# Performance work log

Measured on AMD Instinct MI355X. Metric: run time of the kernel, lower is better.

Reference implementation:

```python
import jax, jax.numpy as jnp
import numpy as np

B, C, N = 32, 128, 64
HID = 2 * C
STEEPNESS = 50.0


def _bitonic_layers(n):
    """Index pairs (a, b) for each compare-exchange layer of a bitonic sorting
    network, matching diffsort's bitonic_network construction."""
    num_blocks = int(np.log2(n))
    assert n == 2 ** num_blocks
    layers = []
    for block in range(num_blocks):
        for layer in range(block + 1):
            m = 2 ** (block - layer)
            a_idx, b_idx = [], []
            for i in range(0, n, 2 * m):
                for j in range(m):
                    ix = i + j
                    a, b = ix, ix + m
                    # alternate direction within bitonic blocks
                    if (ix // 2 ** (block + 1)) % 2 == 1:
                        a, b = b, a
                    a_idx.append(a)
                    b_idx.append(b)
            layers.append((np.asarray(a_idx), np.asarray(b_idx)))
    return layers

_LAYERS = _bitonic_layers(N)  # 21 layers for N=64


def _diff_sort(scores):
    """Differentiable bitonic sort (diffsort, distribution='cauchy').
    Returns (soft-sorted scores, soft permutation matrix P) with
    sorted = scores @ P; the module applies P via bmm(P, rows)."""
    b, n = scores.shape
    x = scores
    P = jnp.broadcast_to(jnp.eye(n, dtype=scores.dtype), (b, n, n))
    inv_pi = 1.0 / np.pi
    for a_idx, b_idx in _LAYERS:
        xa, xb = x[:, a_idx], x[:, b_idx]
        alpha = jnp.arctan((xb - xa) * STEEPNESS) * inv_pi + 0.5  # Cauchy CDF
        x = x.at[:, a_idx].set(alpha * xa + (1.0 - alpha) * xb)
        x = x.at[:, b_idx].set((1.0 - alpha) * xa + alpha * xb)
        Pa, Pb = P[:, :, a_idx], P[:, :, b_idx]
        al = alpha[:, None, :]
        P = P.at[:, :, a_idx].set(al * Pa + (1.0 - al) * Pb)
        P = P.at[:, :, b_idx].set((1.0 - al) * Pa + al * Pb)
    return x, P


def setup_inputs() -> dict:
    key = jax.random.key(0)
    ks = jax.random.split(key, 9)
    s = 0.05  # keep score magnitudes reasonable under steepness=50
    return {
        "x": jax.random.normal(ks[0], (B, C, N, N), jnp.float32),
        "w1": jax.random.normal(ks[1], (HID, C), jnp.float32) * s,
        "b1": jax.random.normal(ks[2], (HID,), jnp.float32) * s,
        "w2": jax.random.normal(ks[3], (HID, HID), jnp.float32) * s,
        "b2": jax.random.normal(ks[4], (HID,), jnp.float32) * s,
        "w_row": jax.random.normal(ks[5], (HID, N), jnp.float32) * s,
        "b_row": jax.random.normal(ks[6], (1,), jnp.float32) * s,
        "w_col": jax.random.normal(ks[7], (HID, N), jnp.float32) * s,
        "b_col": jax.random.normal(ks[8], (1,), jnp.float32) * s,
    }


def reference(x, w1, b1, w2, b2, w_row, b_row, w_col, b_col):
    # feat_extractor: two 1x1 convs (pointwise channel GEMMs) + ReLU
    h = jax.nn.relu(jnp.einsum('bchw,oc->bohw', x, w1) + b1[None, :, None, None])
    h = jax.nn.relu(jnp.einsum('bchw,oc->bohw', h, w2) + b2[None, :, None, None])

    # row branch: Conv1d(HID*N,1,1) over flattened (channel, width) per row
    row_scores = jnp.einsum('bchw,cw->bh', h, w_row) + b_row  # (B, N)
    _, p_row = _diff_sort(row_scores)
    x = jnp.einsum('bij,bcjk->bcik', p_row, x)  # bmm(P_row, x) per channel

    # col branch: Conv1d(HID*N,1,1) over flattened (channel, height) per column
    col_scores = jnp.einsum('bchw,ch->bw', h, w_col) + b_col  # (B, N)
    _, p_col = _diff_sort(col_scores)
    # original: bmm(P_col, x^T) then view as (B,C,N,N) with NO transpose back
    x = jnp.einsum('bij,bckj->bcik', p_col, x)
    return x
```

## Files before the change

### kernel.cpp

```cpp
#include <hip/hip_runtime.h>
#include <math.h>

#define B_    32
#define C_    128
#define N_    64
#define HID_  256
#define PIX_  4096
#define STEEP 50.0f
#define INV_PI 0.318309886183790671f
#define LDA   40
#define LDX   72

typedef unsigned short u16;
typedef __attribute__((ext_vector_type(8))) short bf16x8;
typedef __attribute__((ext_vector_type(4))) float f32x4;

__device__ __forceinline__ u16 f2bf(float f) {
    unsigned int u = __builtin_bit_cast(unsigned int, f);
    unsigned int r = (u + 0x7FFFu + ((u >> 16) & 1u)) >> 16;
    return (u16)r;
}
__device__ __forceinline__ float bf2f(u16 h) {
    unsigned int u = ((unsigned int)h) << 16;
    return __builtin_bit_cast(float, u);
}

__global__ void k0_init(float* __restrict__ row_s, float* __restrict__ col_s,
                        const float* __restrict__ b_row, const float* __restrict__ b_col) {
    int i = blockIdx.x * 256 + threadIdx.x;
    if (i < B_ * N_) row_s[i] = b_row[0];
    else {
        int j = i - B_ * N_;
        if (j < B_ * N_) col_s[j] = b_col[0];
    }
}

__global__ void k_prep(const float* __restrict__ w1, const float* __restrict__ w2,
                       u16* __restrict__ w1h, u16* __restrict__ w1l,
                       u16* __restrict__ w2h, u16* __restrict__ w2l) {
    int i = blockIdx.x * 256 + threadIdx.x;
    if (i < HID_ * C_) {
        float v = w1[i];
        u16 h = f2bf(v);
        w1h[i] = h;
        w1l[i] = f2bf(v - bf2f(h));
    } else {
        int j = i - HID_ * C_;
        if (j < HID_ * HID_) {
            float v = w2[j];
            u16 h = f2bf(v);
            w2h[j] = h;
            w2l[j] = f2bf(v - bf2f(h));
        }
    }
}

__global__ __launch_bounds__(256) void k1_conv1(const float* __restrict__ x,
                                                const u16* __restrict__ w1h,
                                                const u16* __restrict__ w1l,
                                                const float* __restrict__ b1,
                                                u16* __restrict__ h1h,
                                                u16* __restrict__ h1l) {
    __shared__ __align__(16) u16 Ah[128 * LDA];
    __shared__ __align__(16) u16 Al[128 * LDA];
    __shared__ __align__(16) u16 Bh[128 * LDA];
    __shared__ __align__(16) u16 Bl[128 * LDA];
    const int t = threadIdx.x;
    const int l = t & 63, wv = t >> 6;
    const int row = l & 15, q = l >> 4;
    const int pbase = blockIdx.x * 128, obase = blockIdx.y * 128, b = blockIdx.z;
    const int mwave = (wv & 1) * 64, nwave = (wv >> 1) * 64;
    const float* xb = x + (size_t)b * C_ * PIX_ + pbase;

    f32x4 acc[4][4];
#pragma unroll
    for (int i = 0; i < 4; i++)
#pragma unroll
        for (int j = 0; j < 4; j++) acc[i][j] = (f32x4){0.f, 0.f, 0.f, 0.f};

    for (int k0 = 0; k0 < C_; k0 += 32) {
        {
            int o = t >> 1, hf = t & 1;
            const float4* sh = (const float4*)&w1h[(size_t)(obase + o) * C_ + k0 + hf * 16];
            const float4* sl = (const float4*)&w1l[(size_t)(obase + o) * C_ + k0 + hf * 16];
            float4 vh0 = sh[0], vh1 = sh[1];
            float4 vl0 = sl[0], vl1 = sl[1];
            *(float4*)&Ah[o * LDA + hf * 16] = vh0;
            *(float4*)&Ah[o * LDA + hf * 16 + 8] = vh1;
            *(float4*)&Al[o * LDA + hf * 16] = vl0;
            *(float4*)&Al[o * LDA + hf * 16 + 8] = vl1;
        }
        {
            int cp = t & 15, pg = t >> 4;
            int c = k0 + cp * 2;
            float4 a0 = *(const float4*)&xb[(size_t)c * PIX_ + pg * 8];
            float4 a1 = *(const float4*)&xb[(size_t)c * PIX_ + pg * 8 + 4];
            float4 c0v = *(const float4*)&xb[(size_t)(c + 1) * PIX_ + pg * 8];
            float4 c1v = *(const float4*)&xb[(size_t)(c + 1) * PIX_ + pg * 8 + 4];
            float va[8] = {a0.x, a0.y, a0.z, a0.w, a1.x, a1.y, a1.z, a1.w};
            float vb[8] = {c0v.x, c0v.y, c0v.z, c0v.w, c1v.x, c1v.y, c1v.z, c1v.w};
#pragma unroll
            for (int j = 0; j < 8; j++) {
                u16 h0 = f2bf(va[j]), h1v = f2bf(vb[j]);
                u16 l0 = f2bf(va[j] - bf2f(h0)), l1 = f2bf(vb[j] - bf2f(h1v));
                *(unsigned int*)&Bh[(pg * 8 + j) * LDA + cp * 2] =
                    (unsigned int)h0 | ((unsigned int)h1v << 16);
                *(unsigned int*)&Bl[(pg * 8 + j) * LDA + cp * 2] =
                    (unsigned int)l0 | ((unsigned int)l1 << 16);
            }
        }
        __syncthreads();

        bf16x8 afh[4], afl[4], bfh[4], bfl[4];
#pragma unroll
        for (int mf = 0; mf < 4; mf++) {
            afh[mf] = *(const bf16x8*)&Ah[(mwave + mf * 16 + row) * LDA + q * 8];
            afl[mf] = *(const bf16x8*)&Al[(mwave + mf * 16 + row) * LDA + q * 8];
        }
#pragma unroll
        for (int nf = 0; nf < 4; nf++) {
            bfh[nf] = *(const bf16x8*)&Bh[(nwave + nf * 16 + row) * LDA + q * 8];
            bfl[nf] = *(const bf16x8*)&Bl[(nwave + nf * 16 + row) * LDA + q * 8];
        }
#pragma unroll
        for (int mf = 0; mf < 4; mf++)
#pragma unroll
            for (int nf = 0; nf < 4; nf++) {
                acc[mf][nf] = __builtin_amdgcn_mfma_f32_16x16x32_bf16(afh[mf], bfh[nf], acc[mf][nf], 0, 0, 0);
                acc[mf][nf] = __builtin_amdgcn_mfma_f32_16x16x32_bf16(afh[mf], bfl[nf], acc[mf][nf], 0, 0, 0);
                acc[mf][nf] = __builtin_amdgcn_mfma_f32_16x16x32_bf16(afl[mf], bfh[nf], acc[mf][nf], 0, 0, 0);
            }
        __syncthreads();
    }

#pragma unroll
    for (int mf = 0; mf < 4; mf++) {
        int o = obase + mwave + mf * 16 + q * 4;
        float bias[4];
#pragma unroll
        for (int r = 0; r < 4; r++) bias[r] = b1[o + r];
#pragma unroll
        for (int nf = 0; nf < 4; nf++) {
            int p = pbase + nwave + nf * 16 + row;
            u16 hh[4], ll[4];
#pragma unroll
            for (int r = 0; r < 4; r++) {
                float v = fmaxf(acc[mf][nf][r] + bias[r], 0.f);
                u16 h = f2bf(v);
                hh[r] = h;
                ll[r] = f2bf(v - bf2f(h));
            }
            size_t base = ((size_t)b * PIX_ + p) * HID_ + o;
            *(unsigned long long*)&h1h[base] =
                (unsigned long long)hh[0] | ((unsigned long long)hh[1] << 16) |
                ((unsigned long long)hh[2] << 32) | ((unsigned long long)hh[3] << 48);
            *(unsigned long long*)&h1l[base] =
                (unsigned long long)ll[0] | ((unsigned long long)ll[1] << 16) |
                ((unsigned long long)ll[2] << 32) | ((unsigned long long)ll[3] << 48);
        }
    }
}

__global__ __launch_bounds__(256) void k2_conv2_scores(
    const u16* __restrict__ h1h, const u16* __restrict__ h1l,
    const u16* __restrict__ w2h, const u16* __restrict__ w2l,
    const float* __restrict__ b2, const float* __restrict__ w_row,
    const float* __restrict__ w_col, float* __restrict__ row_s,
    float* __restrict__ col_s) {
    __shared__ __align__(16) u16 Ah[128 * LDA];
    __shared__ __align__(16) u16 Al[128 * LDA];
    __shared__ __align__(16) u16 Bh[128 * LDA];
    __shared__ __align__(16) u16 Bl[128 * LDA];
    __shared__ float col_red[64];
    __shared__ float row_red[2];
    const int t = threadIdx.x;
    const int l = t & 63, wv = t >> 6;
    const int row = l & 15, q = l >> 4;
    const int pbase = blockIdx.x * 128, obase = blockIdx.y * 128, b = blockIdx.z;
    const int mwave = (wv & 1) * 64, nwave = (wv >> 1) * 64;

    if (t < 64) col_red[t] = 0.f;
    if (t < 2) row_red[t] = 0.f;

    f32x4 acc[4][4];
#pragma unroll
    for (int i = 0; i < 4; i++)
#pragma unroll
        for (int j = 0; j < 4; j++) acc[i][j] = (f32x4){0.f, 0.f, 0.f, 0.f};

    for (int k0 = 0; k0 < HID_; k0 += 32) {
        {
            int o = t >> 1, hf = t & 1;
            const float4* sh = (const float4*)&w2h[(size_t)(obase + o) * HID_ + k0 + hf * 16];
            const float4* sl = (const float4*)&w2l[(size_t)(obase + o) * HID_ + k0 + hf * 16];
            float4 vh0 = sh[0], vh1 = sh[1];
            float4 vl0 = sl[0], vl1 = sl[1];
            *(float4*)&Ah[o * LDA + hf * 16] = vh0;
            *(float4*)&Ah[o * LDA + hf * 16 + 8] = vh1;
            *(float4*)&Al[o * LDA + hf * 16] = vl0;
            *(float4*)&Al[o * LDA + hf * 16 + 8] = vl1;
        }
        {
            int p = t >> 1, hf = t & 1;
            size_t base = ((size_t)b * PIX_ + pbase + p) * HID_ + k0 + hf * 16;
            const float4* sh = (const float4*)&h1h[base];
            const float4* sl = (const float4*)&h1l[base];
            float4 vh0 = sh[0], vh1 = sh[1];
            float4 vl0 = sl[0], vl1 = sl[1];
            *(float4*)&Bh[p * LDA + hf * 16] = vh0;
            *(float4*)&Bh[p * LDA + hf * 16 + 8] = vh1;
            *(float4*)&Bl[p * LDA + hf * 16] = vl0;
            *(float4*)&Bl[p * LDA + hf * 16 + 8] = vl1;
        }
        __syncthreads();

        bf16x8 afh[4], afl[4], bfh[4], bfl[4];
#pragma unroll
        for (int mf = 0; mf < 4; mf++) {
            afh[mf] = *(const bf16x8*)&Ah[(mwave + mf * 16 + row) * LDA + q * 8];
            afl[mf] = *(const bf16x8*)&Al[(mwave + mf * 16 + row) * LDA + q * 8];
        }
#pragma unroll
        for (int nf = 0; nf < 4; nf++) {
            bfh[nf] = *(const bf16x8*)&Bh[(nwave + nf * 16 + row) * LDA + q * 8];
            bfl[nf] = *(const bf16x8*)&Bl[(nwave + nf * 16 + row) * LDA + q * 8];
        }
#pragma unroll
        for (int mf = 0; mf < 4; mf++)
#pragma unroll
            for (int nf = 0; nf < 4; nf++) {
                acc[mf][nf] = __builtin_amdgcn_mfma_f32_16x16x32_bf16(afh[mf], bfh[nf], acc[mf][nf], 0, 0, 0);
                acc[mf][nf] = __builtin_amdgcn_mfma_f32_16x16x32_bf16(afh[mf], bfl[nf], acc[mf][nf], 0, 0, 0);
                acc[mf][nf] = __builtin_amdgcn_mfma_f32_16x16x32_bf16(afl[mf], bfh[nf], acc[mf][nf], 0, 0, 0);
            }
        __syncthreads();
    }

    const int h0 = pbase >> 6;
    const int h = h0 + (wv >> 1);
    float rpart = 0.f;
    float cpart[4] = {0.f, 0.f, 0.f, 0.f};
#pragma unroll
    for (int mf = 0; mf < 4; mf++) {
        int o = obase + mwave + mf * 16 + q * 4;
#pragma unroll
        for (int r = 0; r < 4; r++) {
            float bias = b2[o + r];
            float wcv = w_col[(o + r) * N_ + h];
#pragma unroll
            for (int nf = 0; nf < 4; nf++) {
                int w = nf * 16 + row;
                float v = fmaxf(acc[mf][nf][r] + bias, 0.f);
                rpart += v * w_row[(o + r) * N_ + w];
                cpart[nf] += v * wcv;
            }
        }
    }
    __syncthreads();
#pragma unroll
    for (int off = 32; off; off >>= 1) rpart += __shfl_xor(rpart, off, 64);
    if (l == 0) atomicAdd(&row_red[wv >> 1], rpart);
#pragma unroll
    for (int nf = 0; nf < 4; nf++) {
        float cp = cpart[nf];
        cp += __shfl_xor(cp, 16, 64);
        cp += __shfl_xor(cp, 32, 64);
        if (l < 16) atomicAdd(&col_red[nf * 16 + l], cp);
    }
    __syncthreads();
    if (t < 64) atomicAdd(&col_s[b * N_ + t], col_red[t]);
    if (t < 2) atomicAdd(&row_s[b * N_ + h0 + t], row_red[t]);
}

__global__ __launch_bounds__(256) void k4_diffsort(const float* __restrict__ row_s,
                                                   const float* __restrict__ col_s,
                                                   u16* __restrict__ prow_h, u16* __restrict__ prow_l,
                                                   u16* __restrict__ pcol_h, u16* __restrict__ pcol_l) {
    __shared__ float Ps[64 * 65];
    __shared__ float xs[64];
    __shared__ float als[32];
    const int t = threadIdx.x;
    const int which = blockIdx.x & 1;
    const int b = blockIdx.x >> 1;
    const float* sc = which ? col_s : row_s;
    u16* Ph = which ? pcol_h : prow_h;
    u16* Pl = which ? pcol_l : prow_l;

    if (t < 64) xs[t] = sc[b * 64 + t];
#pragma unroll
    for (int k = 0; k < 16; k++) {
        int idx = t + k * 256;
        int i = idx >> 6, j = idx & 63;
        Ps[i * 65 + j] = (i == j) ? 1.f : 0.f;
    }
    __syncthreads();

    const int r = t & 63, pg = t >> 6;
    for (int bl = 0; bl < 6; bl++) {
        for (int ly = 0; ly <= bl; ly++) {
            int sh = bl - ly;
            int m = 1 << sh;
            if (t < 32) {
                int i = (t >> sh) << (sh + 1);
                int j = t & (m - 1);
                int ix = i + j;
                int a = ix, bi = ix + m;
                if ((ix >> (bl + 1)) & 1) { int tmp = a; a = bi; bi = tmp; }
                float xa = xs[a], xbv = xs[bi];
                float al = atanf((xbv - xa) * STEEP) * INV_PI + 0.5f;
                als[t] = al;
                xs[a] = al * xa + (1.f - al) * xbv;
                xs[bi] = (1.f - al) * xa + al * xbv;
            }
            __syncthreads();
#pragma unroll
            for (int pi = 0; pi < 8; pi++) {
                int p = pg * 8 + pi;
                int i = (p >> sh) << (sh + 1);
                int j = p & (m - 1);
                int ix = i + j;
                int a = ix, bi = ix + m;
                if ((ix >> (bl + 1)) & 1) { int tmp = a; a = bi; bi = tmp; }
                float al = als[p];
                float Pa = Ps[r * 65 + a], Pb = Ps[r * 65 + bi];
                Ps[r * 65 + a] = al * Pa + (1.f - al) * Pb;
                Ps[r * 65 + bi] = (1.f - al) * Pa + al * Pb;
            }
            __syncthreads();
        }
    }
#pragma unroll
    for (int k = 0; k < 16; k++) {
        int idx = t + k * 256;
        int i = idx >> 6, j = idx & 63;
        float v = Ps[i * 65 + j];
        u16 h = f2bf(v);
        Ph[b * 4096 + idx] = h;
        Pl[b * 4096 + idx] = f2bf(v - bf2f(h));
    }
}

__global__ __launch_bounds__(256) void k5_permute(const float* __restrict__ x,
                                                  const u16* __restrict__ pcol_h,
                                                  const u16* __restrict__ pcol_l,
                                                  const u16* __restrict__ prow_h,
                                                  const u16* __restrict__ prow_l,
                                                  float* __restrict__ out) {
    __shared__ __align__(16) u16 Xh[64 * LDX];
    __shared__ __align__(16) u16 Xl[64 * LDX];
    __shared__ __align__(16) u16 Zh[64 * LDX];
    __shared__ __align__(16) u16 Zl[64 * LDX];
    const int t = threadIdx.x;
    const int l = t & 63, w = t >> 6;
    const int col = l & 15, q = l >> 4;
    const int b = blockIdx.y;
    const int cbase = blockIdx.x * 4;
    const int i0 = w * 16;

    const u16* pch = pcol_h + (size_t)b * 4096;
    const u16* pcl = pcol_l + (size_t)b * 4096;
    const u16* prh = prow_h + (size_t)b * 4096;
    const u16* prl = prow_l + (size_t)b * 4096;

    bf16x8 pcA_h[2], pcA_l[2];
#pragma unroll
    for (int ks = 0; ks < 2; ks++) {
        pcA_h[ks] = *(const bf16x8*)&pch[(i0 + col) * 64 + q * 8 + ks * 32];
        pcA_l[ks] = *(const bf16x8*)&pcl[(i0 + col) * 64 + q * 8 + ks * 32];
    }

    for (int ci = 0; ci < 4; ci++) {
        const int c = cbase + ci;
        const float* xc = x + ((size_t)b * C_ + c) * PIX_;
#pragma unroll
        for (int k = 0; k < 4; k++) {
            int f = t + k * 256;
            int rw = f >> 4, c4 = f & 15;
            float4 v = *(const float4*)&xc[f * 4];
            u16 h0 = f2bf(v.x), h1 = f2bf(v.y), h2 = f2bf(v.z), h3 = f2bf(v.w);
            ushort4 hv = {h0, h1, h2, h3};
            ushort4 lv = {f2bf(v.x - bf2f(h0)), f2bf(v.y - bf2f(h1)),
                          f2bf(v.z - bf2f(h2)), f2bf(v.w - bf2f(h3))};
            *(ushort4*)&Xh[rw * LDX + c4 * 4] = hv;
            *(ushort4*)&Xl[rw * LDX + c4 * 4] = lv;
        }
        __syncthreads();

        f32x4 acc[4];
#pragma unroll
        for (int nt = 0; nt < 4; nt++) acc[nt] = (f32x4){0.f, 0.f, 0.f, 0.f};
#pragma unroll
        for (int ks = 0; ks < 2; ks++) {
            bf16x8 ah = pcA_h[ks], al_ = pcA_l[ks];
#pragma unroll
            for (int nt = 0; nt < 4; nt++) {
                bf16x8 bh = *(const bf16x8*)&Xh[(nt * 16 + col) * LDX + q * 8 + ks * 32];
                bf16x8 bl = *(const bf16x8*)&Xl[(nt * 16 + col) * LDX + q * 8 + ks * 32];
                acc[nt] = __builtin_amdgcn_mfma_f32_16x16x32_bf16(ah, bh, acc[nt], 0, 0, 0);
                acc[nt] = __builtin_amdgcn_mfma_f32_16x16x32_bf16(ah, bl, acc[nt], 0, 0, 0);
                acc[nt] = __builtin_amdgcn_mfma_f32_16x16x32_bf16(al_, bh, acc[nt], 0, 0, 0);
            }
        }
#pragma unroll
        for (int nt = 0; nt < 4; nt++)
#pragma unroll
            for (int r = 0; r < 4; r++) {
                float v = acc[nt][r];
                u16 h = f2bf(v);
                int rw = i0 + q * 4 + r;
                Zh[rw * LDX + nt * 16 + col] = h;
                Zl[rw * LDX + nt * 16 + col] = f2bf(v - bf2f(h));
            }

        f32x4 acc2[4];
#pragma unroll
        for (int nt = 0; nt < 4; nt++) acc2[nt] = (f32x4){0.f, 0.f, 0.f, 0.f};
#pragma unroll
        for (int ks = 0; ks < 2; ks++) {
            bf16x8 ah = *(const bf16x8*)&Zh[(i0 + col) * LDX + q * 8 + ks * 32];
            bf16x8 al_ = *(const bf16x8*)&Zl[(i0 + col) * LDX + q * 8 + ks * 32];
#pragma unroll
            for (int nt = 0; nt < 4; nt++) {
                bf16x8 bh = *(const bf16x8*)&prh[(nt * 16 + col) * 64 + q * 8 + ks * 32];
                bf16x8 bl = *(const bf16x8*)&prl[(nt * 16 + col) * 64 + q * 8 + ks * 32];
                acc2[nt] = __builtin_amdgcn_mfma_f32_16x16x32_bf16(ah, bh, acc2[nt], 0, 0, 0);
                acc2[nt] = __builtin_amdgcn_mfma_f32_16x16x32_bf16(ah, bl, acc2[nt], 0, 0, 0);
                acc2[nt] = __builtin_amdgcn_mfma_f32_16x16x32_bf16(al_, bh, acc2[nt], 0, 0, 0);
            }
        }
        float* oc = out + ((size_t)b * C_ + c) * PIX_;
#pragma unroll
        for (int nt = 0; nt < 4; nt++)
#pragma unroll
            for (int r = 0; r < 4; r++)
                oc[(i0 + q * 4 + r) * 64 + nt * 16 + col] = acc2[nt][r];
        __syncthreads();
    }
}

extern "C" void kernel_launch(void* const* d_in, const int* in_sizes, int n_in,
                              void* d_out, int out_size, void* d_ws, size_t ws_size,
                              hipStream_t stream) {
    const float* x = (const float*)d_in[0];
    const float* w1 = (const float*)d_in[1];
    const float* b1 = (const float*)d_in[2];
    const float* w2 = (const float*)d_in[3];
    const float* b2 = (const float*)d_in[4];
    const float* w_row = (const float*)d_in[5];
    const float* b_row = (const float*)d_in[6];
    const float* w_col = (const float*)d_in[7];
    const float* b_col = (const float*)d_in[8];
    float* out = (float*)d_out;

    char* ws = (char*)d_ws;
    u16* h1h = (u16*)(ws);
    u16* h1l = (u16*)(ws + 67108864);
    u16* w1h = (u16*)(ws + 134217728);
    u16* w1l = (u16*)(ws + 134283264);
    u16* w2h = (u16*)(ws + 134348800);
    u16* w2l = (u16*)(ws + 134479872);
    float* row_s = (float*)(ws + 134610944);
    float* col_s = (float*)(ws + 134619136);
    u16* prow_h = (u16*)(ws + 134627328);
    u16* prow_l = (u16*)(ws + 134889472);
    u16* pcol_h = (u16*)(ws + 135151616);
    u16* pcol_l = (u16*)(ws + 135413760);

    hipLaunchKernelGGL(k0_init, dim3(16), dim3(256), 0, stream, row_s, col_s, b_row, b_col);
    hipLaunchKernelGGL(k_prep, dim3(384), dim3(256), 0, stream, w1, w2, w1h, w1l, w2h, w2l);
    hipLaunchKernelGGL(k1_conv1, dim3(32, 2, 32), dim3(256), 0, stream, x, w1h, w1l, b1, h1h, h1l);
    hipLaunchKernelGGL(k2_conv2_scores, dim3(32, 2, 32), dim3(256), 0, stream,
                       h1h, h1l, w2h, w2l, b2, w_row, w_col, row_s, col_s);
    hipLaunchKernelGGL(k4_diffsort, dim3(64), dim3(256), 0, stream,
                       row_s, col_s, prow_h, prow_l, pcol_h, pcol_l);
    hipLaunchKernelGGL(k5_permute, dim3(32, 32), dim3(256), 0, stream,
                       x, pcol_h, pcol_l, prow_h, prow_l, out);
}
```

Measured before the change: 320.2 us.

## Fuse conv1 and conv2+scores into one kernel keeping h1 in LDS

Merges the two pointwise-conv GEMM kernels into one. Each block handles one image row (64 pixels) across all 256 hidden channels and keeps the split-bf16 intermediate h1 in shared memory, so the 128 MB global write and read of h1 is removed. Weights are now read straight from global memory into MFMA fragments instead of being staged in LDS. Each block computes its row score whole, so the row-score init and its atomics are dropped. The cost is about 70 KB of LDS per block, which lowers occupancy, plus uncached-through-LDS weight loads.

```diff
diff --git a/kernel.cpp b/kernel.cpp
--- a/kernel.cpp
+++ b/kernel.cpp
@@ -9,6 +9,7 @@
 #define STEEP 50.0f
 #define INV_PI 0.318309886183790671f
 #define LDA   40
+#define LDH   272
 #define LDX   72
 
 typedef unsigned short u16;
@@ -25,14 +26,9 @@
     return __builtin_bit_cast(float, u);
 }
 
-__global__ void k0_init(float* __restrict__ row_s, float* __restrict__ col_s,
-                        const float* __restrict__ b_row, const float* __restrict__ b_col) {
+__global__ void k0_init(float* __restrict__ col_s, const float* __restrict__ b_col) {
     int i = blockIdx.x * 256 + threadIdx.x;
-    if (i < B_ * N_) row_s[i] = b_row[0];
-    else {
-        int j = i - B_ * N_;
-        if (j < B_ * N_) col_s[j] = b_col[0];
-    }
+    if (i < B_ * N_) col_s[i] = b_col[0];
 }
 
 __global__ void k_prep(const float* __restrict__ w1, const float* __restrict__ w2,
@@ -55,221 +51,170 @@
     }
 }
 
-__global__ __launch_bounds__(256) void k1_conv1(const float* __restrict__ x,
-                                                const u16* __restrict__ w1h,
-                                                const u16* __restrict__ w1l,
-                                                const float* __restrict__ b1,
-                                                u16* __restrict__ h1h,
-                                                u16* __restrict__ h1l) {
-    __shared__ __align__(16) u16 Ah[128 * LDA];
-    __shared__ __align__(16) u16 Al[128 * LDA];
-    __shared__ __align__(16) u16 Bh[128 * LDA];
-    __shared__ __align__(16) u16 Bl[128 * LDA];
+__global__ __launch_bounds__(256) void k12_fused(
+    const float* __restrict__ x,
+    const u16* __restrict__ w1h, const u16* __restrict__ w1l,
+    const float* __restrict__ b1,
+    const u16* __restrict__ w2h, const u16* __restrict__ w2l,
+    const float* __restrict__ b2, const float* __restrict__ w_row,
+    const float* __restrict__ b_row, const float* __restrict__ w_col,
+    float* __restrict__ row_s, float* __restrict__ col_s) {
+    __shared__ __align__(16) u16 Lh1h[64 * LDH];
+    __shared__ __align__(16) u16 Lh1l[64 * LDH];
+    __shared__ __align__(16) u16 Bh[64 * LDA];
+    __shared__ __align__(16) u16 Bl[64 * LDA];
+    __shared__ float col_red[64];
+    __shared__ float row_red;
+
     const int t = threadIdx.x;
-    const int l = t & 63, wv = t >> 6;
-    const int row = l & 15, q = l >> 4;
-    const int pbase = blockIdx.x * 128, obase = blockIdx.y * 128, b = blockIdx.z;
-    const int mwave = (wv & 1) * 64, nwave = (wv >> 1) * 64;
+    const int l = t & 63, w = t >> 6;
+    const int col = l & 15, q = l >> 4;
+    const int hrow = blockIdx.x;
+    const int b = blockIdx.y;
+    const int pbase = hrow * 64;
     const float* xb = x + (size_t)b * C_ * PIX_ + pbase;
 
+    if (t < 64) col_red[t] = 0.f;
+    if (t == 0) row_red = 0.f;
+
     f32x4 acc[4][4];
 #pragma unroll
     for (int i = 0; i < 4; i++)
 #pragma unroll
         for (int j = 0; j < 4; j++) acc[i][j] = (f32x4){0.f, 0.f, 0.f, 0.f};
 
-    for (int k0 = 0; k0 < C_; k0 += 32) {
+    const int pt = t & 15, ct = t >> 4;
+    for (int kc = 0; kc < 4; kc++) {
+        const int c0 = kc * 32;
         {
-            int o = t >> 1, hf = t & 1;
-            const float4* sh = (const float4*)&w1h[(size_t)(obase + o) * C_ + k0 + hf * 16];
-            const float4* sl = (const float4*)&w1l[(size_t)(obase + o) * C_ + k0 + hf * 16];
-            float4 vh0 = sh[0], vh1 = sh[1];
-            float4 vl0 = sl[0], vl1 = sl[1];
-            *(float4*)&Ah[o * LDA + hf * 16] = vh0;
-            *(float4*)&Ah[o * LDA + hf * 16 + 8] = vh1;
-            *(float4*)&Al[o * LDA + hf * 16] = vl0;
-            *(float4*)&Al[o * LDA + hf * 16 + 8] = vl1;
-        }
-        {
-            int cp = t & 15, pg = t >> 4;
-            int c = k0 + cp * 2;
-            float4 a0 = *(const float4*)&xb[(size_t)c * PIX_ + pg * 8];
-            float4 a1 = *(const float4*)&xb[(size_t)c * PIX_ + pg * 8 + 4];
-            float4 c0v = *(const float4*)&xb[(size_t)(c + 1) * PIX_ + pg * 8];
-            float4 c1v = *(const float4*)&xb[(size_t)(c + 1) * PIX_ + pg * 8 + 4];
-            float va[8] = {a0.x, a0.y, a0.z, a0.w, a1.x, a1.y, a1.z, a1.w};
-            float vb[8] = {c0v.x, c0v.y, c0v.z, c0v.w, c1v.x, c1v.y, c1v.z, c1v.w};
-#pragma unroll
-            for (int j = 0; j < 8; j++) {
-                u16 h0 = f2bf(va[j]), h1v = f2bf(vb[j]);
-                u16 l0 = f2bf(va[j] - bf2f(h0)), l1 = f2bf(vb[j] - bf2f(h1v));
-                *(unsigned int*)&Bh[(pg * 8 + j) * LDA + cp * 2] =
-                    (unsigned int)h0 | ((unsigned int)h1v << 16);
-                *(unsigned int*)&Bl[(pg * 8 + j) * LDA + cp * 2] =
+            const float* r0 = &xb[(size_t)(c0 + 2 * ct) * PIX_ + pt * 4];
+            const float* r1 = &xb[(size_t)(c0 + 2 * ct + 1) * PIX_ + pt * 4];
+            float4 v0 = *(const float4*)r0;
+            float4 v1 = *(const float4*)r1;
+            float a0[4] = {v0.x, v0.y, v0.z, v0.w};
+            float a1[4] = {v1.x, v1.y, v1.z, v1.w};
+#pragma unroll
+            for (int j = 0; j < 4; j++) {
+                u16 h0 = f2bf(a0[j]), h1 = f2bf(a1[j]);
+                u16 l0 = f2bf(a0[j] - bf2f(h0)), l1 = f2bf(a1[j] - bf2f(h1));
+                *(unsigned int*)&Bh[(pt * 4 + j) * LDA + 2 * ct] =
+                    (unsigned int)h0 | ((unsigned int)h1 << 16);
+                *(unsigned int*)&Bl[(pt * 4 + j) * LDA + 2 * ct] =
                     (unsigned int)l0 | ((unsigned int)l1 << 16);
             }
         }
         __syncthreads();
-
-        bf16x8 afh[4], afl[4], bfh[4], bfl[4];
+        bf16x8 ah[4], al_[4], bh[4], bl[4];
 #pragma unroll
         for (int mf = 0; mf < 4; mf++) {
-            afh[mf] = *(const bf16x8*)&Ah[(mwave + mf * 16 + row) * LDA + q * 8];
-            afl[mf] = *(const bf16x8*)&Al[(mwave + mf * 16 + row) * LDA + q * 8];
-        }
-#pragma unroll
-        for (int nf = 0; nf < 4; nf++) {
-            bfh[nf] = *(const bf16x8*)&Bh[(nwave + nf * 16 + row) * LDA + q * 8];
-            bfl[nf] = *(const bf16x8*)&Bl[(nwave + nf * 16 + row) * LDA + q * 8];
+            size_t ro = (size_t)(64 * w + 16 * mf + col) * C_ + c0 + q * 8;
+            ah[mf] = *(const bf16x8*)&w1h[ro];
+            al_[mf] = *(const bf16x8*)&w1l[ro];
+        }
+#pragma unroll
+        for (int nt = 0; nt < 4; nt++) {
+            bh[nt] = *(const bf16x8*)&Bh[(nt * 16 + col) * LDA + q * 8];
+            bl[nt] = *(const bf16x8*)&Bl[(nt * 16 + col) * LDA + q * 8];
         }
 #pragma unroll
         for (int mf = 0; mf < 4; mf++)
 #pragma unroll
-            for (int nf = 0; nf < 4; nf++) {
-                acc[mf][nf] = __builtin_amdgcn_mfma_f32_16x16x32_bf16(afh[mf], bfh[nf], acc[mf][nf], 0, 0, 0);
-                acc[mf][nf] = __builtin_amdgcn_mfma_f32_16x16x32_bf16(afh[mf], bfl[nf], acc[mf][nf], 0, 0, 0);
-                acc[mf][nf] = __builtin_amdgcn_mfma_f32_16x16x32_bf16(afl[mf], bfh[nf], acc[mf][nf], 0, 0, 0);
+            for (int nt = 0; nt < 4; nt++) {
+                acc[mf][nt] = __builtin_amdgcn_mfma_f32_16x16x32_bf16(ah[mf], bh[nt], acc[mf][nt], 0, 0, 0);
+                acc[mf][nt] = __builtin_amdgcn_mfma_f32_16x16x32_bf16(ah[mf], bl[nt], acc[mf][nt], 0, 0, 0);
+                acc[mf][nt] = __builtin_amdgcn_mfma_f32_16x16x32_bf16(al_[mf], bh[nt], acc[mf][nt], 0, 0, 0);
             }
         __syncthreads();
     }
 
 #pragma unroll
     for (int mf = 0; mf < 4; mf++) {
-        int o = obase + mwave + mf * 16 + q * 4;
+        int o = 64 * w + 16 * mf + q * 4;
         float bias[4];
 #pragma unroll
         for (int r = 0; r < 4; r++) bias[r] = b1[o + r];
 #pragma unroll
-        for (int nf = 0; nf < 4; nf++) {
-            int p = pbase + nwave + nf * 16 + row;
+        for (int nt = 0; nt < 4; nt++) {
+            int p = nt * 16 + col;
             u16 hh[4], ll[4];
 #pragma unroll
             for (int r = 0; r < 4; r++) {
-                float v = fmaxf(acc[mf][nf][r] + bias[r], 0.f);
+                float v = fmaxf(acc[mf][nt][r] + bias[r], 0.f);
                 u16 h = f2bf(v);
                 hh[r] = h;
                 ll[r] = f2bf(v - bf2f(h));
             }
-            size_t base = ((size_t)b * PIX_ + p) * HID_ + o;
-            *(unsigned long long*)&h1h[base] =
+            *(unsigned long long*)&Lh1h[p * LDH + o] =
                 (unsigned long long)hh[0] | ((unsigned long long)hh[1] << 16) |
                 ((unsigned long long)hh[2] << 32) | ((unsigned long long)hh[3] << 48);
-            *(unsigned long long*)&h1l[base] =
+            *(unsigned long long*)&Lh1l[p * LDH + o] =
                 (unsigned long long)ll[0] | ((unsigned long long)ll[1] << 16) |
                 ((unsigned long long)ll[2] << 32) | ((unsigned long long)ll[3] << 48);
         }
     }
-}
-
-__global__ __launch_bounds__(256) void k2_conv2_scores(
-    const u16* __restrict__ h1h, const u16* __restrict__ h1l,
-    const u16* __restrict__ w2h, const u16* __restrict__ w2l,
-    const float* __restrict__ b2, const float* __restrict__ w_row,
-    const float* __restrict__ w_col, float* __restrict__ row_s,
-    float* __restrict__ col_s) {
-    __shared__ __align__(16) u16 Ah[128 * LDA];
-    __shared__ __align__(16) u16 Al[128 * LDA];
-    __shared__ __align__(16) u16 Bh[128 * LDA];
-    __shared__ __align__(16) u16 Bl[128 * LDA];
-    __shared__ float col_red[64];
-    __shared__ float row_red[2];
-    const int t = threadIdx.x;
-    const int l = t & 63, wv = t >> 6;
-    const int row = l & 15, q = l >> 4;
-    const int pbase = blockIdx.x * 128, obase = blockIdx.y * 128, b = blockIdx.z;
-    const int mwave = (wv & 1) * 64, nwave = (wv >> 1) * 64;
-
-    if (t < 64) col_red[t] = 0.f;
-    if (t < 2) row_red[t] = 0.f;
-
-    f32x4 acc[4][4];
+    __syncthreads();
+
+    f32x4 acc2[4][4];
 #pragma unroll
     for (int i = 0; i < 4; i++)
 #pragma unroll
-        for (int j = 0; j < 4; j++) acc[i][j] = (f32x4){0.f, 0.f, 0.f, 0.f};
-
-    for (int k0 = 0; k0 < HID_; k0 += 32) {
-        {
-            int o = t >> 1, hf = t & 1;
-            const float4* sh = (const float4*)&w2h[(size_t)(obase + o) * HID_ + k0 + hf * 16];
-            const float4* sl = (const float4*)&w2l[(size_t)(obase + o) * HID_ + k0 + hf * 16];
-            float4 vh0 = sh[0], vh1 = sh[1];
-            float4 vl0 = sl[0], vl1 = sl[1];
-            *(float4*)&Ah[o * LDA + hf * 16] = vh0;
-            *(float4*)&Ah[o * LDA + hf * 16 + 8] = vh1;
-            *(float4*)&Al[o * LDA + hf * 16] = vl0;
-            *(float4*)&Al[o * LDA + hf * 16 + 8] = vl1;
-        }
-        {
-            int p = t >> 1, hf = t & 1;
-            size_t base = ((size_t)b * PIX_ + pbase + p) * HID_ + k0 + hf * 16;
-            const float4* sh = (const float4*)&h1h[base];
-            const float4* sl = (const float4*)&h1l[base];
-            float4 vh0 = sh[0], vh1 = sh[1];
-            float4 vl0 = sl[0], vl1 = sl[1];
-            *(float4*)&Bh[p * LDA + hf * 16] = vh0;
-            *(float4*)&Bh[p * LDA + hf * 16 + 8] = vh1;
-            *(float4*)&Bl[p * LDA + hf * 16] = vl0;
-            *(float4*)&Bl[p * LDA + hf * 16 + 8] = vl1;
-        }
-        __syncthreads();
-
-        bf16x8 afh[4], afl[4], bfh[4], bfl[4];
+        for (int j = 0; j < 4; j++) acc2[i][j] = (f32x4){0.f, 0.f, 0.f, 0.f};
+
+    for (int kc = 0; kc < 8; kc++) {
+        const int k0 = kc * 32;
+        bf16x8 ah[4], al_[4], bh[4], bl[4];
 #pragma unroll
         for (int mf = 0; mf < 4; mf++) {
-            afh[mf] = *(const bf16x8*)&Ah[(mwave + mf * 16 + row) * LDA + q * 8];
-            afl[mf] = *(const bf16x8*)&Al[(mwave + mf * 16 + row) * LDA + q * 8];
-        }
-#pragma unroll
-        for (int nf = 0; nf < 4; nf++) {
-            bfh[nf] = *(const bf16x8*)&Bh[(nwave + nf * 16 + row) * LDA + q * 8];
-            bfl[nf] = *(const bf16x8*)&Bl[(nwave + nf * 16 + row) * LDA + q * 8];
+            size_t ro = (size_t)(64 * w + 16 * mf + col) * HID_ + k0 + q * 8;
+            ah[mf] = *(const bf16x8*)&w2h[ro];
+            al_[mf] = *(const bf16x8*)&w2l[ro];
+        }
+#pragma unroll
+        for (int nt = 0; nt < 4; nt++) {
+            bh[nt] = *(const bf16x8*)&Lh1h[(nt * 16 + col) * LDH + k0 + q * 8];
+            bl[nt] = *(const bf16x8*)&Lh1l[(nt * 16 + col) * LDH + k0 + q * 8];
         }
 #pragma unroll
         for (int mf = 0; mf < 4; mf++)
 #pragma unroll
-            for (int nf = 0; nf < 4; nf++) {
-                acc[mf][nf] = __builtin_amdgcn_mfma_f32_16x16x32_bf16(afh[mf], bfh[nf], acc[mf][nf], 0, 0, 0);
-                acc[mf][nf] = __builtin_amdgcn_mfma_f32_16x16x32_bf16(afh[mf], bfl[nf], acc[mf][nf], 0, 0, 0);
-                acc[mf][nf] = __builtin_amdgcn_mfma_f32_16x16x32_bf16(afl[mf], bfh[nf], acc[mf][nf], 0, 0, 0);
-            }
-        __syncthreads();
-    }
-
-    const int h0 = pbase >> 6;
-    const int h = h0 + (wv >> 1);
+            for (int nt = 0; nt < 4; nt++) {
+                acc2[mf][nt] = __builtin_amdgcn_mfma_f32_16x16x32_bf16(ah[mf], bh[nt], acc2[mf][nt], 0, 0, 0);
+                acc2[mf][nt] = __builtin_amdgcn_mfma_f32_16x16x32_bf16(ah[mf], bl[nt], acc2[mf][nt], 0, 0, 0);
+                acc2[mf][nt] = __builtin_amdgcn_mfma_f32_16x16x32_bf16(al_[mf], bh[nt], acc2[mf][nt], 0, 0, 0);
+            }
+    }
+
     float rpart = 0.f;
     float cpart[4] = {0.f, 0.f, 0.f, 0.f};
 #pragma unroll
     for (int mf = 0; mf < 4; mf++) {
-        int o = obase + mwave + mf * 16 + q * 4;
+        int o = 64 * w + 16 * mf + q * 4;
 #pragma unroll
         for (int r = 0; r < 4; r++) {
             float bias = b2[o + r];
-            float wcv = w_col[(o + r) * N_ + h];
-#pragma unroll
-            for (int nf = 0; nf < 4; nf++) {
-                int w = nf * 16 + row;
-                float v = fmaxf(acc[mf][nf][r] + bias, 0.f);
-                rpart += v * w_row[(o + r) * N_ + w];
-                cpart[nf] += v * wcv;
-            }
-        }
-    }
-    __syncthreads();
+            float wcv = w_col[(o + r) * N_ + hrow];
+#pragma unroll
+            for (int nt = 0; nt < 4; nt++) {
+                int wc = nt * 16 + col;
+                float v = fmaxf(acc2[mf][nt][r] + bias, 0.f);
+                rpart += v * w_row[(o + r) * N_ + wc];
+                cpart[nt] += v * wcv;
+            }
+        }
+    }
 #pragma unroll
     for (int off = 32; off; off >>= 1) rpart += __shfl_xor(rpart, off, 64);
-    if (l == 0) atomicAdd(&row_red[wv >> 1], rpart);
-#pragma unroll
-    for (int nf = 0; nf < 4; nf++) {
-        float cp = cpart[nf];
+    if (l == 0) atomicAdd(&row_red, rpart);
+#pragma unroll
+    for (int nt = 0; nt < 4; nt++) {
+        float cp = cpart[nt];
         cp += __shfl_xor(cp, 16, 64);
         cp += __shfl_xor(cp, 32, 64);
-        if (l < 16) atomicAdd(&col_red[nf * 16 + l], cp);
+        if (l < 16) atomicAdd(&col_red[nt * 16 + l], cp);
     }
     __syncthreads();
     if (t < 64) atomicAdd(&col_s[b * N_ + t], col_red[t]);
-    if (t < 2) atomicAdd(&row_s[b * N_ + h0 + t], row_red[t]);
+    if (t == 0) row_s[b * N_ + hrow] = b_row[0] + row_red;
 }
 
 __global__ __launch_bounds__(256) void k4_diffsort(const float* __restrict__ row_s,
@@ -453,24 +398,21 @@
     float* out = (float*)d_out;
 
     char* ws = (char*)d_ws;
-    u16* h1h = (u16*)(ws);
-    u16* h1l = (u16*)(ws + 67108864);
-    u16* w1h = (u16*)(ws + 134217728);
-    u16* w1l = (u16*)(ws + 134283264);
-    u16* w2h = (u16*)(ws + 134348800);
-    u16* w2l = (u16*)(ws + 134479872);
-    float* row_s = (float*)(ws + 134610944);
-    float* col_s = (float*)(ws + 134619136);
-    u16* prow_h = (u16*)(ws + 134627328);
-    u16* prow_l = (u16*)(ws + 134889472);
-    u16* pcol_h = (u16*)(ws + 135151616);
-    u16* pcol_l = (u16*)(ws + 135413760);
-
-    hipLaunchKernelGGL(k0_init, dim3(16), dim3(256), 0, stream, row_s, col_s, b_row, b_col);
+    u16* w1h = (u16*)(ws);
+    u16* w1l = (u16*)(ws + 65536);
+    u16* w2h = (u16*)(ws + 131072);
+    u16* w2l = (u16*)(ws + 262144);
+    float* row_s = (float*)(ws + 393216);
+    float* col_s = (float*)(ws + 401408);
+    u16* prow_h = (u16*)(ws + 409600);
+    u16* prow_l = (u16*)(ws + 671744);
+    u16* pcol_h = (u16*)(ws + 933888);
+    u16* pcol_l = (u16*)(ws + 1196032);
+
+    hipLaunchKernelGGL(k0_init, dim3(8), dim3(256), 0, stream, col_s, b_col);
     hipLaunchKernelGGL(k_prep, dim3(384), dim3(256), 0, stream, w1, w2, w1h, w1l, w2h, w2l);
-    hipLaunchKernelGGL(k1_conv1, dim3(32, 2, 32), dim3(256), 0, stream, x, w1h, w1l, b1, h1h, h1l);
-    hipLaunchKernelGGL(k2_conv2_scores, dim3(32, 2, 32), dim3(256), 0, stream,
-                       h1h, h1l, w2h, w2l, b2, w_row, w_col, row_s, col_s);
+    hipLaunchKernelGGL(k12_fused, dim3(64, 32), dim3(256), 0, stream,
+                       x, w1h, w1l, b1, w2h, w2l, b2, w_row, b_row, w_col, row_s, col_s);
     hipLaunchKernelGGL(k4_diffsort, dim3(64), dim3(256), 0, stream,
                        row_s, col_s, prow_h, prow_l, pcol_h, pcol_l);
     hipLaunchKernelGGL(k5_permute, dim3(32, 32), dim3(256), 0, stream,
```

After: 292.5 us. -8.7%, faster.
